# Optimization experiments

Measured on AMD Instinct MI355X. Metric: run time of the kernel, lower is better.

Reference implementation:

```python
import jax, jax.numpy as jnp
import numpy as np

V, E, H = 100000, 128, 128  # vocab, embed_dim, lstm_units per direction
B, T = 128, 512             # batch, seq_len


def setup_inputs() -> dict:
    key = jax.random.key(0)
    ks = jax.random.split(key, 16)
    s = 0.05
    x = jax.random.randint(ks[0], (B, T), 0, V)
    emb_table = jax.random.normal(ks[1], (V, E), dtype=jnp.float32) * s
    emb_table = emb_table.at[0].set(0.0)  # padding_idx=0
    def w(k, shape):
        return jax.random.normal(k, shape, dtype=jnp.float32) * s
    return {
        "x": x,
        "emb_table": emb_table,
        "Wih_f": w(ks[2], (4 * H, E)), "Whh_f": w(ks[3], (4 * H, H)),
        "bih_f": w(ks[4], (4 * H,)),  "bhh_f": w(ks[5], (4 * H,)),
        "Wih_b": w(ks[6], (4 * H, E)), "Whh_b": w(ks[7], (4 * H, H)),
        "bih_b": w(ks[8], (4 * H,)),  "bhh_b": w(ks[9], (4 * H,)),
        "W1": w(ks[10], (64, 2 * H)), "b1": w(ks[11], (64,)),
        "W2": w(ks[12], (1, 64)),     "b2": w(ks[13], (1,)),
    }


def _lstm_scan(xp, Whh):
    """xp: (T, B, 4H) precomputed input projection (+biases). Returns hs: (T, B, H)."""
    Hd = Whh.shape[1]

    def step(carry, gx):
        h, c = carry
        g = gx + h @ Whh.T                      # (B, 4H)
        i, f, gg, o = jnp.split(g, 4, axis=-1)  # PyTorch gate order: i, f, g, o
        i = jax.nn.sigmoid(i)
        f = jax.nn.sigmoid(f)
        gg = jnp.tanh(gg)
        o = jax.nn.sigmoid(o)
        c = f * c + i * gg
        h = o * jnp.tanh(c)
        return (h, c), h

    h0 = jnp.zeros((xp.shape[1], Hd), xp.dtype)
    _, hs = jax.lax.scan(step, (h0, h0), xp)
    return hs


def reference(x, emb_table, Wih_f, Whh_f, bih_f, bhh_f,
              Wih_b, Whh_b, bih_b, bhh_b, W1, b1, W2, b2):
    emb = emb_table[x]                                      # (B, T, E)
    # forward direction: precompute input projections for all timesteps
    xp_f = jnp.einsum('bte,ge->tbg', emb, Wih_f) + bih_f + bhh_f  # (T, B, 4H)
    hs_f = _lstm_scan(xp_f, Whh_f)                           # (T, B, H)
    # backward direction: run on time-reversed sequence, then reverse outputs
    xp_b = jnp.einsum('bte,ge->tbg', emb[:, ::-1, :], Wih_b) + bih_b + bhh_b
    hs_b = _lstm_scan(xp_b, Whh_b)[::-1]                     # (T, B, H)
    lstm_out = jnp.concatenate([hs_f, hs_b], axis=-1)        # (T, B, 2H)
    pooled = jnp.max(lstm_out, axis=0)                       # (B, 2H) max over time
    h1 = jax.nn.relu(pooled @ W1.T + b1)                     # dropout = identity (eval)
    return jax.nn.sigmoid(h1 @ W2.T + b2)                    # (B, 1)
```

## Files before the change

### kernel.cpp

```cpp
#include <hip/hip_runtime.h>
#include <hip/hip_fp16.h>

#define TT 512
#define HH 128

typedef _Float16 half2_t __attribute__((ext_vector_type(2)));
typedef _Float16 half4_t __attribute__((ext_vector_type(4)));
typedef _Float16 half8_t __attribute__((ext_vector_type(8)));
typedef float    float4_t __attribute__((ext_vector_type(4)));

__device__ __forceinline__ half2_t h2(float v) {
    half2_t r; r[0] = (_Float16)v; r[1] = (_Float16)v; return r;
}
__device__ __forceinline__ half2_t pkrtz(float a, float b) {
    return __builtin_bit_cast(half2_t, __builtin_amdgcn_cvt_pkrtz(a, b));
}

#define TC1 0.994940f
#define TC3 -0.290799f
#define TC5 0.065507f
#define TC7 -0.0062464f
#define SC1 0.2487350f
#define SC3 -0.0181749f
#define SC5 0.00102355f
#define SC7 -0.0000244141f

__device__ __forceinline__ half2_t tanh_pk(half2_t x) {
    half2_t m = __builtin_elementwise_min(__builtin_elementwise_max(x, h2(-2.0f)), h2(2.0f));
    half2_t t = m * m;
    half2_t p = h2(TC7) * t + h2(TC5);
    p = p * t + h2(TC3);
    p = p * t + h2(TC1);
    return m * p;
}
__device__ __forceinline__ half2_t sigma_pk(half2_t x) {
    half2_t m = __builtin_elementwise_min(__builtin_elementwise_max(x, h2(-4.0f)), h2(4.0f));
    half2_t t = m * m;
    half2_t p = h2(SC7) * t + h2(SC5);
    p = p * t + h2(SC3);
    p = p * t + h2(SC1);
    return m * p + h2(0.5f);
}

__device__ __forceinline__ void wg_barrier_lds() {
#if __has_builtin(__builtin_amdgcn_s_waitcnt)
    __builtin_amdgcn_s_waitcnt(0xC07F);
#else
    asm volatile("s_waitcnt lgkmcnt(0)" ::: "memory");
#endif
    __builtin_amdgcn_s_barrier();
}

__device__ __forceinline__ size_t xp_off(int dirbg, int t, int w, int lane) {
    return (((size_t)dirbg * 512 + t) * 8 + w) * 1024 + (size_t)lane * 16;
}

__global__ __attribute__((amdgpu_flat_work_group_size(512, 512), amdgpu_waves_per_eu(2, 2)))
void xp_gemm_kernel(
    const int* __restrict__ x, const float* __restrict__ emb,
    const float* __restrict__ Wih_f, const float* __restrict__ bih_f, const float* __restrict__ bhh_f,
    const float* __restrict__ Wih_b, const float* __restrict__ bih_b, const float* __restrict__ bhh_b,
    _Float16* __restrict__ xp)
{
    const int wg  = blockIdx.x;
    const int dir = wg >> 3, bg = wg & 7;
    const int tb  = blockIdx.y * 16;

    const float* Wih = dir ? Wih_b : Wih_f;
    const float* bih = dir ? bih_b : bih_f;
    const float* bhh = dir ? bhh_b : bhh_f;

    const int tid = threadIdx.x;
    const int w = tid >> 6, lane = tid & 63, lq = lane >> 4, lm = lane & 15;

    __shared__ int id_sm[16 * 16];
    if (tid < 256) {
        int i = tid >> 4, j = tid & 15;
        id_sm[i * 16 + j] = x[(size_t)(bg * 16 + i) * TT + tb + j];
    }

    half8_t awih[4][4];
    #pragma unroll
    for (int T = 0; T < 4; ++T) {
        #pragma unroll
        for (int kk = 0; kk < 4; ++kk) {
            const float4* s = (const float4*)(Wih + (size_t)(T * 128 + w * 16 + lm) * 128 + kk * 32 + lq * 8);
            float4 v0 = s[0], v1 = s[1];
            half8_t h;
            half2_t a = pkrtz(v0.x, v0.y), b = pkrtz(v0.z, v0.w);
            half2_t c = pkrtz(v1.x, v1.y), d = pkrtz(v1.z, v1.w);
            h[0]=a[0]; h[1]=a[1]; h[2]=b[0]; h[3]=b[1];
            h[4]=c[0]; h[5]=c[1]; h[6]=d[0]; h[7]=d[1];
            awih[T][kk] = h;
        }
    }
    float4_t biasv[4];
    #pragma unroll
    for (int T = 0; T < 4; ++T) {
        int g = T * 128 + w * 16 + lq * 4;
        float4 b1 = *(const float4*)(bih + g);
        float4 b2 = *(const float4*)(bhh + g);
        biasv[T] = (float4_t){b1.x + b2.x, b1.y + b2.y, b1.z + b2.z, b1.w + b2.w};
    }
    __syncthreads();

    half8_t EF[2][4];
    {
        int id = id_sm[lm * 16 + 0];
        const float* base = emb + (size_t)id * 128 + lq * 8;
        #pragma unroll
        for (int kk = 0; kk < 4; ++kk) {
            float4 v0 = *(const float4*)(base + kk * 32);
            float4 v1 = *(const float4*)(base + kk * 32 + 4);
            half8_t h;
            half2_t a = pkrtz(v0.x, v0.y), b = pkrtz(v0.z, v0.w);
            half2_t c = pkrtz(v1.x, v1.y), d = pkrtz(v1.z, v1.w);
            h[0]=a[0]; h[1]=a[1]; h[2]=b[0]; h[3]=b[1];
            h[4]=c[0]; h[5]=c[1]; h[6]=d[0]; h[7]=d[1];
            EF[0][kk] = h;
        }
    }

    #pragma unroll
    for (int i = 0; i < 16; ++i) {
        const int cur = i & 1;
        float4 rv[8];
        if (i + 1 < 16) {
            int id = id_sm[lm * 16 + i + 1];
            const float* base = emb + (size_t)id * 128 + lq * 8;
            #pragma unroll
            for (int kk = 0; kk < 4; ++kk) {
                rv[2 * kk]     = *(const float4*)(base + kk * 32);
                rv[2 * kk + 1] = *(const float4*)(base + kk * 32 + 4);
            }
        }

        float4_t acc[4];
        #pragma unroll
        for (int T = 0; T < 4; ++T) acc[T] = biasv[T];
        #pragma unroll
        for (int kk = 0; kk < 4; ++kk)
            #pragma unroll
            for (int T = 0; T < 4; ++T)
                acc[T] = __builtin_amdgcn_mfma_f32_16x16x32_f16(awih[T][kk], EF[cur][kk], acc[T], 0, 0, 0);

        half8_t p0, p1;
        {
            half2_t a = pkrtz(acc[0][0], acc[0][1]), b = pkrtz(acc[0][2], acc[0][3]);
            half2_t c = pkrtz(acc[1][0], acc[1][1]), d = pkrtz(acc[1][2], acc[1][3]);
            p0[0]=a[0]; p0[1]=a[1]; p0[2]=b[0]; p0[3]=b[1];
            p0[4]=c[0]; p0[5]=c[1]; p0[6]=d[0]; p0[7]=d[1];
        }
        {
            half2_t a = pkrtz(acc[2][0], acc[2][1]), b = pkrtz(acc[2][2], acc[2][3]);
            half2_t c = pkrtz(acc[3][0], acc[3][1]), d = pkrtz(acc[3][2], acc[3][3]);
            p1[0]=a[0]; p1[1]=a[1]; p1[2]=b[0]; p1[3]=b[1];
            p1[4]=c[0]; p1[5]=c[1]; p1[6]=d[0]; p1[7]=d[1];
        }
        half8_t* dst = (half8_t*)(xp + xp_off(wg, tb + i, w, lane));
        dst[0] = p0; dst[1] = p1;

        if (i + 1 < 16) {
            #pragma unroll
            for (int kk = 0; kk < 4; ++kk) {
                half2_t a = pkrtz(rv[2*kk].x, rv[2*kk].y), b = pkrtz(rv[2*kk].z, rv[2*kk].w);
                half2_t c = pkrtz(rv[2*kk+1].x, rv[2*kk+1].y), d = pkrtz(rv[2*kk+1].z, rv[2*kk+1].w);
                half8_t h;
                h[0]=a[0]; h[1]=a[1]; h[2]=b[0]; h[3]=b[1];
                h[4]=c[0]; h[5]=c[1]; h[6]=d[0]; h[7]=d[1];
                EF[1 - cur][kk] = h;
            }
        }
    }
}

__global__ __attribute__((amdgpu_flat_work_group_size(512, 512), amdgpu_waves_per_eu(2, 2)))
void bilstm_rec_kernel(
    const _Float16* __restrict__ xp,
    const float* __restrict__ Whh_f, const float* __restrict__ Whh_b,
    float* __restrict__ pooled)
{
    const int wg  = blockIdx.x;
    const int dir = wg >> 3, bg = wg & 7;
    const float* Whh = dir ? Whh_b : Whh_f;

    const int tid = threadIdx.x;
    const int w = tid >> 6, lane = tid & 63, lq = lane >> 4, lm = lane & 15;

    __shared__ _Float16 hsm[2][16 * 136];

    half8_t awhh[4][4];
    #pragma unroll
    for (int T = 0; T < 4; ++T) {
        #pragma unroll
        for (int kk = 0; kk < 4; ++kk) {
            const float4* s = (const float4*)(Whh + (size_t)(T * 128 + w * 16 + lm) * 128 + kk * 32 + lq * 8);
            float4 v0 = s[0], v1 = s[1];
            half8_t h;
            half2_t a = pkrtz(v0.x, v0.y), b = pkrtz(v0.z, v0.w);
            half2_t c = pkrtz(v1.x, v1.y), d = pkrtz(v1.z, v1.w);
            h[0]=a[0]; h[1]=a[1]; h[2]=b[0]; h[3]=b[1];
            h[4]=c[0]; h[5]=c[1]; h[6]=d[0]; h[7]=d[1];
            awhh[T][kk] = h;
        }
    }

    for (int k = tid; k < 2 * 16 * 136; k += 512)
        ((_Float16*)hsm)[k] = (_Float16)0.0f;

    const _Float16* xp_wl = xp + ((size_t)wg * 512 * 8 + w) * 1024 + (size_t)lane * 16;

    half8_t Qa[4], Qb[4];
    {
        int ta = dir ? (TT - 1) : 0;
        const half8_t* p = (const half8_t*)(xp_wl + (size_t)ta * 8192);
        Qa[0] = p[0]; Qb[0] = p[1];
    }
    {
        int ta = dir ? (TT - 2) : 1;
        const half8_t* p = (const half8_t*)(xp_wl + (size_t)ta * 8192);
        Qa[1] = p[0]; Qb[1] = p[1];
    }
    __syncthreads();

    half2_t c01 = h2(0.0f), c23 = h2(0.0f);
    half2_t hm01 = h2(-60000.0f), hm23 = h2(-60000.0f);

    for (int tbs = 0; tbs < TT; tbs += 4) {
        #pragma unroll
        for (int P = 0; P < 4; ++P) {
            const int t = tbs + P;
            {
                int tl = (t + 2 < TT) ? (t + 2) : (TT - 1);
                int ta = dir ? (TT - 1 - tl) : tl;
                const half8_t* pp = (const half8_t*)(xp_wl + (size_t)ta * 8192);
                Qa[(P + 2) & 3] = pp[0]; Qb[(P + 2) & 3] = pp[1];
            }

            half8_t bh[4];
            #pragma unroll
            for (int kk = 0; kk < 4; ++kk)
                bh[kk] = *(const half8_t*)&hsm[P & 1][lm * 136 + kk * 32 + lq * 8];

            float4_t acc[4];
            acc[0] = (float4_t){(float)Qa[P][0], (float)Qa[P][1], (float)Qa[P][2], (float)Qa[P][3]};
            acc[1] = (float4_t){(float)Qa[P][4], (float)Qa[P][5], (float)Qa[P][6], (float)Qa[P][7]};
            acc[2] = (float4_t){(float)Qb[P][0], (float)Qb[P][1], (float)Qb[P][2], (float)Qb[P][3]};
            acc[3] = (float4_t){(float)Qb[P][4], (float)Qb[P][5], (float)Qb[P][6], (float)Qb[P][7]};
            #pragma unroll
            for (int kk = 0; kk < 4; ++kk)
                #pragma unroll
                for (int T = 0; T < 4; ++T)
                    acc[T] = __builtin_amdgcn_mfma_f32_16x16x32_f16(awhh[T][kk], bh[kk], acc[T], 0, 0, 0);

            half2_t i01 = sigma_pk(pkrtz(acc[0][0], acc[0][1]));
            half2_t i23 = sigma_pk(pkrtz(acc[0][2], acc[0][3]));
            half2_t f01 = sigma_pk(pkrtz(acc[1][0], acc[1][1]));
            half2_t f23 = sigma_pk(pkrtz(acc[1][2], acc[1][3]));
            half2_t g01 = tanh_pk(pkrtz(acc[2][0], acc[2][1]));
            half2_t g23 = tanh_pk(pkrtz(acc[2][2], acc[2][3]));
            half2_t o01 = sigma_pk(pkrtz(acc[3][0], acc[3][1]));
            half2_t o23 = sigma_pk(pkrtz(acc[3][2], acc[3][3]));

            c01 = f01 * c01 + i01 * g01;
            c23 = f23 * c23 + i23 * g23;
            half2_t h01 = o01 * tanh_pk(c01);
            half2_t h23 = o23 * tanh_pk(c23);
            hm01 = __builtin_elementwise_max(hm01, h01);
            hm23 = __builtin_elementwise_max(hm23, h23);

            half4_t hv4;
            hv4[0] = h01[0]; hv4[1] = h01[1]; hv4[2] = h23[0]; hv4[3] = h23[1];
            *(half4_t*)&hsm[1 - (P & 1)][lm * 136 + w * 16 + lq * 4] = hv4;

            wg_barrier_lds();
        }
    }

    float4 o;
    o.x = (float)hm01[0]; o.y = (float)hm01[1];
    o.z = (float)hm23[0]; o.w = (float)hm23[1];
    *(float4*)&pooled[(size_t)(bg * 16 + lm) * 256 + dir * HH + w * 16 + lq * 4] = o;
}

__global__ __launch_bounds__(64) void mlp_kernel(
    const float* __restrict__ pooled, const float* __restrict__ W1,
    const float* __restrict__ b1, const float* __restrict__ W2,
    const float* __restrict__ b2, float* __restrict__ out)
{
    const int b = blockIdx.x;
    const int j = threadIdx.x;
    const float4* p = (const float4*)(pooled + (size_t)b * 256);
    const float4* wv = (const float4*)(W1 + (size_t)j * 256);
    float s = 0.0f;
    #pragma unroll
    for (int q = 0; q < 64; ++q) {
        float4 pv = p[q];
        float4 ww = wv[q];
        s += pv.x * ww.x + pv.y * ww.y + pv.z * ww.z + pv.w * ww.w;
    }
    s += b1[j];
    s = fmaxf(s, 0.0f);
    float v = W2[j] * s;
    #pragma unroll
    for (int off = 32; off; off >>= 1) v += __shfl_down(v, off);
    if (j == 0) out[b] = 1.0f / (1.0f + __expf(-(v + b2[0])));
}

extern "C" void kernel_launch(void* const* d_in, const int* in_sizes, int n_in,
                              void* d_out, int out_size, void* d_ws, size_t ws_size,
                              hipStream_t stream) {
    const int*   x     = (const int*)d_in[0];
    const float* emb   = (const float*)d_in[1];
    const float* Wih_f = (const float*)d_in[2];
    const float* Whh_f = (const float*)d_in[3];
    const float* bih_f = (const float*)d_in[4];
    const float* bhh_f = (const float*)d_in[5];
    const float* Wih_b = (const float*)d_in[6];
    const float* Whh_b = (const float*)d_in[7];
    const float* bih_b = (const float*)d_in[8];
    const float* bhh_b = (const float*)d_in[9];
    const float* W1    = (const float*)d_in[10];
    const float* b1    = (const float*)d_in[11];
    const float* W2    = (const float*)d_in[12];
    const float* b2    = (const float*)d_in[13];
    float* out = (float*)d_out;

    char* ws = (char*)d_ws;
    float*    pooled = (float*)ws;
    _Float16* xp     = (_Float16*)(ws + 131072);

    hipLaunchKernelGGL(xp_gemm_kernel, dim3(16, 32), dim3(512), 0, stream,
                       x, emb, Wih_f, bih_f, bhh_f, Wih_b, bih_b, bhh_b, xp);
    hipLaunchKernelGGL(bilstm_rec_kernel, dim3(16), dim3(512), 0, stream,
                       xp, Whh_f, Whh_b, pooled);
    hipLaunchKernelGGL(mlp_kernel, dim3(128), dim3(64), 0, stream,
                       pooled, W1, b1, W2, b2, out);
}
```

Measured before the change: 533.9 us.

## Stage embedding tile in shared memory once instead of per-wave redundant gathers

The input-projection GEMM kernel now gathers all 256 embedding rows for its tile cooperatively into LDS as fp16, with each thread loading half a row, and then reads MFMA B fragments from LDS. Previously each of the 8 waves re-gathered the same embedding rows from global memory, software-pipelined with register double-buffering. This cuts redundant global traffic eightfold but adds about 70KB of LDS, an extra barrier, and a serialized load phase before any compute.

```diff
diff --git a/kernel.cpp b/kernel.cpp
--- a/kernel.cpp
+++ b/kernel.cpp
@@ -73,10 +73,11 @@
     const int tid = threadIdx.x;
     const int w = tid >> 6, lane = tid & 63, lq = lane >> 4, lm = lane & 15;
 
-    __shared__ int id_sm[16 * 16];
+    __shared__ int id_sm[256];
+    __shared__ _Float16 Esm[256 * 136];
+
     if (tid < 256) {
-        int i = tid >> 4, j = tid & 15;
-        id_sm[i * 16 + j] = x[(size_t)(bg * 16 + i) * TT + tb + j];
+        id_sm[tid] = x[(size_t)(bg * 16 + (tid >> 4)) * TT + tb + (tid & 15)];
     }
 
     half8_t awih[4][4];
@@ -104,36 +105,30 @@
     }
     __syncthreads();
 
-    half8_t EF[2][4];
     {
-        int id = id_sm[lm * 16 + 0];
-        const float* base = emb + (size_t)id * 128 + lq * 8;
-        #pragma unroll
-        for (int kk = 0; kk < 4; ++kk) {
-            float4 v0 = *(const float4*)(base + kk * 32);
-            float4 v1 = *(const float4*)(base + kk * 32 + 4);
-            half8_t h;
-            half2_t a = pkrtz(v0.x, v0.y), b = pkrtz(v0.z, v0.w);
-            half2_t c = pkrtz(v1.x, v1.y), d = pkrtz(v1.z, v1.w);
-            h[0]=a[0]; h[1]=a[1]; h[2]=b[0]; h[3]=b[1];
-            h[4]=c[0]; h[5]=c[1]; h[6]=d[0]; h[7]=d[1];
-            EF[0][kk] = h;
-        }
-    }
-
-    #pragma unroll
+        const int r  = tid >> 1;
+        const int hf = tid & 1;
+        const int chain = r >> 4, tt = r & 15;
+        const float* src = emb + (size_t)id_sm[r] * 128 + hf * 64;
+        float4 v[16];
+        #pragma unroll
+        for (int j = 0; j < 16; ++j) v[j] = *(const float4*)(src + 4 * j);
+        _Float16* dst = &Esm[(tt * 16 + chain) * 136 + hf * 64];
+        #pragma unroll
+        for (int j = 0; j < 16; ++j) {
+            half2_t a = pkrtz(v[j].x, v[j].y), b = pkrtz(v[j].z, v[j].w);
+            half4_t q; q[0]=a[0]; q[1]=a[1]; q[2]=b[0]; q[3]=b[1];
+            *(half4_t*)(dst + 4 * j) = q;
+        }
+    }
+    __syncthreads();
+
+    #pragma unroll 4
     for (int i = 0; i < 16; ++i) {
-        const int cur = i & 1;
-        float4 rv[8];
-        if (i + 1 < 16) {
-            int id = id_sm[lm * 16 + i + 1];
-            const float* base = emb + (size_t)id * 128 + lq * 8;
-            #pragma unroll
-            for (int kk = 0; kk < 4; ++kk) {
-                rv[2 * kk]     = *(const float4*)(base + kk * 32);
-                rv[2 * kk + 1] = *(const float4*)(base + kk * 32 + 4);
-            }
-        }
+        half8_t bfr[4];
+        #pragma unroll
+        for (int kk = 0; kk < 4; ++kk)
+            bfr[kk] = *(const half8_t*)&Esm[(i * 16 + lm) * 136 + kk * 32 + lq * 8];
 
         float4_t acc[4];
         #pragma unroll
@@ -142,7 +137,7 @@
         for (int kk = 0; kk < 4; ++kk)
             #pragma unroll
             for (int T = 0; T < 4; ++T)
-                acc[T] = __builtin_amdgcn_mfma_f32_16x16x32_f16(awih[T][kk], EF[cur][kk], acc[T], 0, 0, 0);
+                acc[T] = __builtin_amdgcn_mfma_f32_16x16x32_f16(awih[T][kk], bfr[kk], acc[T], 0, 0, 0);
 
         half8_t p0, p1;
         {
@@ -159,18 +154,6 @@
         }
         half8_t* dst = (half8_t*)(xp + xp_off(wg, tb + i, w, lane));
         dst[0] = p0; dst[1] = p1;
-
-        if (i + 1 < 16) {
-            #pragma unroll
-            for (int kk = 0; kk < 4; ++kk) {
-                half2_t a = pkrtz(rv[2*kk].x, rv[2*kk].y), b = pkrtz(rv[2*kk].z, rv[2*kk].w);
-                half2_t c = pkrtz(rv[2*kk+1].x, rv[2*kk+1].y), d = pkrtz(rv[2*kk+1].z, rv[2*kk+1].w);
-                half8_t h;
-                h[0]=a[0]; h[1]=a[1]; h[2]=b[0]; h[3]=b[1];
-                h[4]=c[0]; h[5]=c[1]; h[6]=d[0]; h[7]=d[1];
-                EF[1 - cur][kk] = h;
-            }
-        }
     }
 }
 
```

Measured after the change: 491.2 us. 1.09x faster.
